# Performance work log

Hardware: AMD Instinct MI355X
Metric: run time of the kernel (lower is better)

Reference implementation:

```python
import jax, jax.numpy as jnp
import numpy as np

N = 100000

def _norm_edges(edge_index, n):
    # add self loops, compute symmetric GCN normalization
    loop = jnp.arange(n, dtype=edge_index.dtype)
    src = jnp.concatenate([edge_index[0], loop])
    dst = jnp.concatenate([edge_index[1], loop])
    deg = jax.ops.segment_sum(jnp.ones_like(dst, dtype=jnp.float32), dst, num_segments=n)
    dinv = jnp.where(deg > 0, deg ** -0.5, 0.0)
    norm = dinv[src] * dinv[dst]
    return src, dst, norm

def _gcn(x, W, b, src, dst, norm, n):
    h = x @ W  # [N, out]
    msg = h[src] * norm[:, None]
    return jax.ops.segment_sum(msg, dst, num_segments=n) + b

def setup_inputs() -> dict:
    key = jax.random.key(0)
    ks = jax.random.split(key, 20)
    E = 3200000
    d_in, d_out = 64, 64
    def w(k, i, o):
        return jax.random.normal(k, (i, o), dtype=jnp.float32) * (1.0 / np.sqrt(i))
    return {
        "x": jax.random.normal(ks[0], (N, d_in), dtype=jnp.float32),
        "t": jax.random.normal(ks[1], (N,), dtype=jnp.float32),
        "edge_index": jax.random.randint(ks[2], (2, E), 0, N, dtype=jnp.int64),
        "W1": w(ks[3], d_in + 1, 64), "b1": jnp.zeros((64,), jnp.float32),
        "W2": w(ks[4], 64, 128), "b2": jnp.zeros((128,), jnp.float32),
        "W3": w(ks[5], 128, 256), "b3": jnp.zeros((256,), jnp.float32),
        "W4": w(ks[6], 256, 128), "b4": jnp.zeros((128,), jnp.float32),
        "F1": w(ks[7], 128, 256), "c1": jnp.zeros((256,), jnp.float32),
        "F2": w(ks[8], 256, 128), "c2": jnp.zeros((128,), jnp.float32),
        "F3": w(ks[9], 128, d_out), "c3": jnp.zeros((d_out,), jnp.float32),
    }

def reference(x, t, edge_index, W1, b1, W2, b2, W3, b3, W4, b4, F1, c1, F2, c2, F3, c3):
    n = x.shape[0]
    src, dst, norm = _norm_edges(edge_index, n)
    h = jnp.concatenate([x, t[:, None]], axis=1)
    h = jax.nn.gelu(_gcn(h, W1, b1, src, dst, norm, n))
    h = jax.nn.gelu(_gcn(h, W2, b2, src, dst, norm, n))
    h = jax.nn.gelu(_gcn(h, W3, b3, src, dst, norm, n))
    h = jax.nn.gelu(_gcn(h, W4, b4, src, dst, norm, n))
    h = jax.nn.gelu(h @ F1 + c1)
    h = jax.nn.gelu(h @ F2 + c2)
    return h @ F3 + c3
```

## Files before the change

### kernel.cpp

```cpp
#include <hip/hip_runtime.h>

static constexpr int BLK = 256;

typedef double d2 __attribute__((ext_vector_type(2)));
typedef int    i4 __attribute__((ext_vector_type(4)));

__device__ __forceinline__ double gelu_d(double v){
  double u = 0.7978845608028654 * (v + 0.044715 * v * v * v);
  return 0.5 * v * (1.0 + tanh(u));
}

__global__ void zero_k(int* __restrict__ a, int n){
  int stride = gridDim.x * blockDim.x;
  for (int i = blockIdx.x*blockDim.x + threadIdx.x; i < n; i += stride) a[i] = 0;
}

__global__ void zeromax_k(unsigned long long* m){
  if (threadIdx.x == 0 && blockIdx.x == 0){
    m[0] = 0ull; m[1] = 0ull; m[2] = 0ull; m[3] = 0ull;
  }
}

__global__ void detect_k(const int* __restrict__ ei, int* __restrict__ flag){
  if (threadIdx.x == 0 && blockIdx.x == 0){
    int zeros = 0;
    for (int i = 0; i < 64; ++i) if (ei[2*i + 1] == 0) ++zeros;
    *flag = (zeros >= 48) ? 1 : 0;
  }
}

__global__ void count_k(const int* __restrict__ ei, int E, const int* __restrict__ flag,
                        int* __restrict__ cnt){
  int is64 = *flag;
  int stride = gridDim.x * blockDim.x;
  for (int e = blockIdx.x*blockDim.x + threadIdx.x; e < E; e += stride){
    int d = is64 ? ei[2*(E + e)] : ei[E + e];
    atomicAdd(&cnt[d], 1);
  }
}

__global__ void dinv_k(const int* __restrict__ cnt, double* __restrict__ dinv, int n){
  int i = blockIdx.x*blockDim.x + threadIdx.x;
  if (i < n){
    double deg = (double)(cnt[i] + 1);
    dinv[i] = 1.0 / sqrt(deg);
  }
}

__global__ __launch_bounds__(256)
void scanA_k(const int* __restrict__ cnt, int* __restrict__ partial, int n, int chunk){
  __shared__ int red[256];
  int b = blockIdx.x;
  int lo = b * chunk, hi = min(n, lo + chunk);
  int s = 0;
  for (int i = lo + threadIdx.x; i < hi; i += 256) s += cnt[i];
  red[threadIdx.x] = s; __syncthreads();
  for (int off = 128; off > 0; off >>= 1){
    if (threadIdx.x < off) red[threadIdx.x] += red[threadIdx.x + off];
    __syncthreads();
  }
  if (threadIdx.x == 0) partial[b] = red[0];
}

__global__ __launch_bounds__(256)
void scanB_k(int* __restrict__ partial, int nb){
  __shared__ int sd[256];
  int tid = threadIdx.x;
  int v = (tid < nb) ? partial[tid] : 0;
  sd[tid] = v; __syncthreads();
  for (int off = 1; off < 256; off <<= 1){
    int t = (tid >= off) ? sd[tid - off] : 0;
    __syncthreads();
    sd[tid] += t;
    __syncthreads();
  }
  if (tid < nb) partial[tid] = sd[tid] - v;
  if (tid == 255) partial[nb] = sd[255];
}

__global__ __launch_bounds__(256)
void scanC_k(const int* __restrict__ cnt, const int* __restrict__ partial,
             int* __restrict__ rp, int n, int chunk, int nb){
  __shared__ int sd[256];
  int b = blockIdx.x;
  int lo = b * chunk, hi = min(n, lo + chunk);
  int run = partial[b];
  for (int base = lo; base < hi; base += 256){
    int i = base + threadIdx.x;
    int v = (i < hi) ? cnt[i] : 0;
    sd[threadIdx.x] = v; __syncthreads();
    for (int off = 1; off < 256; off <<= 1){
      int t = (threadIdx.x >= off) ? sd[threadIdx.x - off] : 0;
      __syncthreads();
      sd[threadIdx.x] += t;
      __syncthreads();
    }
    if (i < hi) rp[i] = run + sd[threadIdx.x] - v;
    run += sd[255];
    __syncthreads();
  }
  if (b == 0 && threadIdx.x == 0) rp[n] = partial[nb];
}

__global__ void scatter_k(const int* __restrict__ ei, int E, const int* __restrict__ flag,
                          const int* __restrict__ rp, int* __restrict__ fill,
                          const double* __restrict__ dinv,
                          int* __restrict__ col, double* __restrict__ val){
  int is64 = *flag;
  int stride = gridDim.x * blockDim.x;
  for (int e = blockIdx.x*blockDim.x + threadIdx.x; e < E; e += stride){
    int s = is64 ? ei[2*e]       : ei[e];
    int d = is64 ? ei[2*(E + e)] : ei[E + e];
    int p = rp[d] + atomicAdd(&fill[d], 1);
    col[p] = s;
    if (val) val[p] = dinv[s];
  }
}

template<typename ST>
__global__ void concat_k(const float* __restrict__ x, const float* __restrict__ t,
                         ST* __restrict__ h0, int n){
  int total = n * 66;
  int stride = gridDim.x * blockDim.x;
  for (int idx = blockIdx.x*blockDim.x + threadIdx.x; idx < total; idx += stride){
    int row = idx / 66;
    int c = idx - row * 66;
    float v = (c < 64) ? x[row*64 + c] : (c == 64 ? t[row] : 0.0f);
    h0[idx] = (ST)v;
  }
}

template<typename ST>
__global__ __launch_bounds__(256, 4)
void gemm_k(const ST* __restrict__ A, int K, int lda,
            const float* __restrict__ W, int NOUT,
            const float* __restrict__ bias,
            ST* __restrict__ C, float* __restrict__ Cf,
            int n, int fuse, unsigned long long* __restrict__ amax)
{
  __shared__ __align__(16) double As[128][18];
  __shared__ __align__(16) double Ws[16][66];
  const int row0 = blockIdx.x * 128;
  const int col0 = blockIdx.y * 64;
  const int tid = threadIdx.x;
  const int tr = tid >> 4, tc = tid & 15;
  const int c0 = 2 * tc;
  double acc[8][4] = {};

  const int sar = tid >> 1;
  const int sak = (tid & 1) * 8;
  const int swr = tid >> 4;
  const int swc = (tid & 15) * 4;

  const int ktiles = (K + 15) / 16;

  double ga[8];
  float  gw[4];

  auto loadA = [&](int k0){
    int gr = row0 + sar;
    if constexpr (sizeof(ST) == 8){
      if (gr < n){
        const double* Ap = (const double*)A + (size_t)gr * lda + k0 + sak;
        #pragma unroll
        for (int g = 0; g < 4; ++g){
          d2 v = *(const d2*)(Ap + 2*g);
          ga[2*g] = v.x; ga[2*g+1] = v.y;
        }
      } else {
        #pragma unroll
        for (int u = 0; u < 8; ++u) ga[u] = 0.0;
      }
    } else {
      const ST* Ap = A + (size_t)gr * lda + k0 + sak;
      #pragma unroll
      for (int u = 0; u < 8; ++u){
        int kg = k0 + sak + u;
        ga[u] = (gr < n && kg < K) ? (double)Ap[u] : 0.0;
      }
    }
  };
  auto loadW = [&](int k0){
    int kg = k0 + swr;
    if (kg < K){
      const float* Wp = W + (size_t)kg * NOUT + col0 + swc;
      #pragma unroll
      for (int g = 0; g < 4; ++g) gw[g] = Wp[g];
    } else {
      #pragma unroll
      for (int g = 0; g < 4; ++g) gw[g] = 0.0f;
    }
  };

  loadA(0);
  loadW(0);

  for (int kt = 0; kt < ktiles; ++kt){
    #pragma unroll
    for (int g = 0; g < 4; ++g){
      d2 v; v.x = ga[2*g]; v.y = ga[2*g+1];
      *(d2*)&As[sar][sak + 2*g] = v;
    }
    {
      d2 v0; v0.x = (double)gw[0]; v0.y = (double)gw[1];
      d2 v1; v1.x = (double)gw[2]; v1.y = (double)gw[3];
      *(d2*)&Ws[swr][swc]     = v0;
      *(d2*)&Ws[swr][swc + 2] = v1;
    }
    __syncthreads();
    if (kt + 1 < ktiles){
      loadA((kt + 1) * 16);
      loadW((kt + 1) * 16);
    }
    #pragma unroll
    for (int kk = 0; kk < 16; kk += 2){
      d2 w0a = *(const d2*)&Ws[kk    ][c0];
      d2 w0b = *(const d2*)&Ws[kk    ][c0 + 32];
      d2 w1a = *(const d2*)&Ws[kk + 1][c0];
      d2 w1b = *(const d2*)&Ws[kk + 1][c0 + 32];
      #pragma unroll
      for (int i = 0; i < 8; ++i){
        d2 av = *(const d2*)&As[tr + 16*i][kk];
        acc[i][0] = fma(av.x, w0a.x, acc[i][0]);
        acc[i][1] = fma(av.x, w0a.y, acc[i][1]);
        acc[i][2] = fma(av.x, w0b.x, acc[i][2]);
        acc[i][3] = fma(av.x, w0b.y, acc[i][3]);
        acc[i][0] = fma(av.y, w1a.x, acc[i][0]);
        acc[i][1] = fma(av.y, w1a.y, acc[i][1]);
        acc[i][2] = fma(av.y, w1b.x, acc[i][2]);
        acc[i][3] = fma(av.y, w1b.y, acc[i][3]);
      }
    }
    __syncthreads();
  }
  double tmax = 0.0;
  #pragma unroll
  for (int i = 0; i < 8; ++i){
    int r = row0 + tr + 16*i;
    if (r >= n) continue;
    #pragma unroll
    for (int j = 0; j < 4; ++j){
      int c = col0 + ((j < 2) ? (c0 + j) : (c0 + 30 + j));
      double v = acc[i][j];
      if (fuse){ v += (double)bias[c]; if (fuse == 1) v = gelu_d(v); }
      if (amax) tmax = fmax(tmax, fabs(v));
      if (fuse == 2) __builtin_nontemporal_store((float)v, &Cf[(size_t)r * NOUT + c]);
      else           __builtin_nontemporal_store((ST)v,   &C [(size_t)r * NOUT + c]);
    }
  }
  if (amax){
    #pragma unroll
    for (int off = 32; off > 0; off >>= 1)
      tmax = fmax(tmax, __shfl_xor(tmax, off));
    if ((threadIdx.x & 63) == 0)
      atomicMax(amax, (unsigned long long)__double_as_longlong(tmax));
  }
}


__global__ void absmaxW_k(const float* __restrict__ W, int n, unsigned long long* __restrict__ out){
  double tmax = 0.0;
  int stride = gridDim.x * blockDim.x;
  for (int i = blockIdx.x*blockDim.x + threadIdx.x; i < n; i += stride)
    tmax = fmax(tmax, (double)fabsf(W[i]));
  #pragma unroll
  for (int off = 32; off > 0; off >>= 1)
    tmax = fmax(tmax, __shfl_xor(tmax, off));
  if ((threadIdx.x & 63) == 0)
    atomicMax(out, (unsigned long long)__double_as_longlong(tmax));
}

__global__ void quantW_k(const float* __restrict__ W, int K, int N,
                         const unsigned long long* __restrict__ maxw,
                         char* __restrict__ WqT){
  double wm = __longlong_as_double((long long)*maxw);
  int sw = (wm > 0.0) ? (37 - ilogb(wm)) : 0;
  double sc = ldexp(1.0, sw);
  int total = K * N;
  size_t NK = (size_t)N * K;
  int stride = gridDim.x * blockDim.x;
  for (int t = blockIdx.x*blockDim.x + threadIdx.x; t < total; t += stride){
    int k = t / N, nn = t - k * N;
    long long v = __double2ll_rn((double)W[t] * sc);
    #pragma unroll
    for (int p = 0; p < 5; ++p){
      int d = (int)((v + 128) & 255) - 128;
      WqT[(size_t)p * NK + (size_t)nn * K + k] = (char)d;
      v = (v - d) >> 8;
    }
  }
}

__global__ __launch_bounds__(512)
void ozaki_k(const double* __restrict__ A, const char* __restrict__ WqT,
             const unsigned long long* __restrict__ maxa,
             const unsigned long long* __restrict__ maxw,
             const float* __restrict__ bias,
             double* __restrict__ C, int n, int fuse)
{
  constexpr int K = 256, N = 128;
  constexpr int PP[22] = {0,0,0, 1,1,1,1, 2,2,2,2,2, 3,3,3,3,3, 4,4,4,4,4};
  constexpr int QQ[22] = {2,3,4, 1,2,3,4, 0,1,2,3,4, 0,1,2,3,4, 0,1,2,3,4};
  __shared__ __align__(16) char laq[5][16][272];
  const int tid  = threadIdx.x;
  const int lane = tid & 63;
  const int ct   = tid >> 6;
  const int l15  = lane & 15;
  const int lk   = lane >> 4;
  const int row0 = blockIdx.x * 16;

  double am = __longlong_as_double((long long)*maxa);
  double wm = __longlong_as_double((long long)*maxw);
  int sa = (am > 0.0) ? (38 - ilogb(am)) : 0;
  int sw = (wm > 0.0) ? (37 - ilogb(wm)) : 0;
  double sc = ldexp(1.0, sa);

  {
    int r  = tid >> 5;
    int k8 = (tid & 31) * 8;
    int gr = row0 + r; if (gr >= n) gr = n - 1;
    const double* Ap = A + (size_t)gr * K + k8;
    unsigned long long pack[5] = {0,0,0,0,0};
    #pragma unroll
    for (int u = 0; u < 8; ++u){
      long long v = __double2ll_rn(Ap[u] * sc);
      #pragma unroll
      for (int p = 0; p < 5; ++p){
        int d = (int)((v + 128) & 255) - 128;
        pack[p] |= (unsigned long long)(unsigned char)d << (8*u);
        v = (v - d) >> 8;
      }
    }
    #pragma unroll
    for (int p = 0; p < 5; ++p)
      *(unsigned long long*)&laq[p][r][k8] = pack[p];
  }
  __syncthreads();

  i4 acc[22];
  #pragma unroll
  for (int i = 0; i < 22; ++i){ i4 z = {0,0,0,0}; acc[i] = z; }

  const size_t NK = (size_t)N * K;
  const char* Wbase = WqT + (size_t)(ct * 16 + l15) * K + lk * 16;
  #pragma unroll
  for (int ks = 0; ks < 4; ++ks){
    int k0 = ks * 64;
    i4 af[5], bf[5];
    #pragma unroll
    for (int p = 0; p < 5; ++p)
      af[p] = *(const i4*)&laq[p][l15][k0 + lk*16];
    #pragma unroll
    for (int q = 0; q < 5; ++q)
      bf[q] = *(const i4*)(Wbase + (size_t)q * NK + k0);
    #pragma unroll
    for (int i = 0; i < 22; ++i)
      acc[i] = __builtin_amdgcn_mfma_i32_16x16x64_i8(af[PP[i]], bf[QQ[i]], acc[i], 0, 0, 0);
  }

  double s = ldexp(1.0, -(sa + sw));
  #pragma unroll
  for (int m = 0; m < 4; ++m){
    int r = row0 + lk * 4 + m;
    if (r >= n) continue;
    double sum = 0.0;
    #pragma unroll
    for (int i = 0; i < 22; ++i)
      sum += ldexp((double)acc[i][m], 8 * (PP[i] + QQ[i]));
    int c = ct * 16 + l15;
    double v = sum * s;
    if (fuse) v = gelu_d(v + (double)bias[c]);
    __builtin_nontemporal_store(v, &C[(size_t)r * N + c]);
  }
}

template<typename ST, int NC>
__global__ __launch_bounds__(256)
void agg_k(const ST* __restrict__ T, const int* __restrict__ rp,
           const int* __restrict__ col, const double* __restrict__ val,
           const double* __restrict__ dinv, const float* __restrict__ bias,
           ST* __restrict__ O, int n, int fuse)
{
  constexpr int DOUT = NC * 64;
  int w = (blockIdx.x * blockDim.x + threadIdx.x) >> 6;
  int lane = threadIdx.x & 63;
  if (w >= n) return;
  double dv = dinv[w];
  const ST* Ti = T + (size_t)w * DOUT;
  double acc[NC];
  #pragma unroll
  for (int c = 0; c < NC; ++c) acc[c] = dv * (double)Ti[lane + 64*c];
  int e  = rp[w];
  int e1 = rp[w + 1];
  if (val){
    for (; e + 4 <= e1; e += 4){
      int s0 = __builtin_nontemporal_load(&col[e]);
      int s1 = __builtin_nontemporal_load(&col[e+1]);
      int s2 = __builtin_nontemporal_load(&col[e+2]);
      int s3 = __builtin_nontemporal_load(&col[e+3]);
      double v0 = __builtin_nontemporal_load(&val[e]);
      double v1 = __builtin_nontemporal_load(&val[e+1]);
      double v2 = __builtin_nontemporal_load(&val[e+2]);
      double v3 = __builtin_nontemporal_load(&val[e+3]);
      const ST* T0 = T + (size_t)s0 * DOUT;
      const ST* T1 = T + (size_t)s1 * DOUT;
      const ST* T2 = T + (size_t)s2 * DOUT;
      const ST* T3 = T + (size_t)s3 * DOUT;
      double t0[NC], t1[NC], t2[NC], t3[NC];
      #pragma unroll
      for (int c = 0; c < NC; ++c){
        t0[c] = (double)T0[lane + 64*c];
        t1[c] = (double)T1[lane + 64*c];
        t2[c] = (double)T2[lane + 64*c];
        t3[c] = (double)T3[lane + 64*c];
      }
      #pragma unroll
      for (int c = 0; c < NC; ++c){
        acc[c] = fma(v0, t0[c], acc[c]);
        acc[c] = fma(v1, t1[c], acc[c]);
        acc[c] = fma(v2, t2[c], acc[c]);
        acc[c] = fma(v3, t3[c], acc[c]);
      }
    }
    for (; e < e1; ++e){
      int s = __builtin_nontemporal_load(&col[e]);
      double v = __builtin_nontemporal_load(&val[e]);
      const ST* Ts = T + (size_t)s * DOUT;
      #pragma unroll
      for (int c = 0; c < NC; ++c) acc[c] = fma(v, (double)Ts[lane + 64*c], acc[c]);
    }
  } else {
    for (; e < e1; ++e){
      int s = col[e];
      double v = dinv[s];
      const ST* Ts = T + (size_t)s * DOUT;
      #pragma unroll
      for (int c = 0; c < NC; ++c) acc[c] = fma(v, (double)Ts[lane + 64*c], acc[c]);
    }
  }
  ST* Oi = O + (size_t)w * DOUT;
  #pragma unroll
  for (int c = 0; c < NC; ++c){
    double v = dv * acc[c];
    if (fuse) v = gelu_d(v + (double)bias[lane + 64*c]);
    __builtin_nontemporal_store((ST)v, &Oi[lane + 64*c]);
  }
}

template<typename ST>
static void run_net(const float* x, const float* t,
                    const float* W1, const float* b1, const float* W2, const float* b2,
                    const float* W3, const float* b3, const float* W4, const float* b4,
                    const float* F1, const float* c1, const float* F2, const float* c2,
                    const float* F3, const float* c3,
                    ST* b256, ST* ba, ST* bb,
                    const int* rp, const int* col, const double* val, const double* dinv,
                    char* Wq4, char* WqF2, unsigned long long* maxbuf, bool ozk,
                    float* out, int N, hipStream_t stream)
{
  auto gemm = [&](const ST* A, int K, int lda, const float* W, int NOUT, const float* bias,
                  ST* C, float* Cf, int fuse, unsigned long long* amax){
    dim3 g((N + 127) / 128, NOUT / 64);
    gemm_k<ST><<<g, dim3(BLK), 0, stream>>>(A, K, lda, W, NOUT, bias, C, Cf, N, fuse, amax);
  };
  int aggGrid = (N * 64 + BLK - 1) / BLK;
  auto agg64 = [&](const ST* T, const float* bias, ST* O, int fuse){
    agg_k<ST,1><<<dim3(aggGrid), dim3(BLK), 0, stream>>>(T, rp, col, val, dinv, bias, O, N, fuse);
  };
  auto agg128 = [&](const ST* T, const float* bias, ST* O, int fuse){
    agg_k<ST,2><<<dim3(aggGrid), dim3(BLK), 0, stream>>>(T, rp, col, val, dinv, bias, O, N, fuse);
  };

  concat_k<ST><<<dim3(1024), dim3(BLK), 0, stream>>>(x, t, ba, N);
  gemm(ba, 65, 66, W1, 64, nullptr, bb, nullptr, 0, nullptr);
  agg64(bb, b1, ba, 1);
  agg64(ba, nullptr, bb, 0);
  gemm(bb, 64, 64, W2, 128, b2, ba, nullptr, 1, nullptr);
  agg128(ba, nullptr, bb, 0);
  gemm(bb, 128, 128, W3, 256, b3, b256, nullptr, 1,
       ozk ? maxbuf : nullptr);
  if (ozk){
    if constexpr (sizeof(ST) == 8){
      ozaki_k<<<dim3((N + 15) / 16), dim3(512), 0, stream>>>(
          (const double*)b256, Wq4, maxbuf, maxbuf + 1, nullptr, (double*)ba, N, 0);
    }
  } else {
    gemm(b256, 256, 256, W4, 128, nullptr, ba, nullptr, 0, nullptr);
  }
  agg128(ba, b4, bb, 1);
  gemm(bb, 128, 128, F1, 256, c1, b256, nullptr, 1,
       ozk ? maxbuf + 2 : nullptr);
  if (ozk){
    if constexpr (sizeof(ST) == 8){
      ozaki_k<<<dim3((N + 15) / 16), dim3(512), 0, stream>>>(
          (const double*)b256, WqF2, maxbuf + 2, maxbuf + 3, c2, (double*)ba, N, 1);
    }
  } else {
    gemm(b256, 256, 256, F2, 128, c2, ba, nullptr, 1, nullptr);
  }
  gemm(ba, 128, 128, F3, 64, c3, nullptr, out, 2, nullptr);
}

extern "C" void kernel_launch(void* const* d_in, const int* in_sizes, int n_in,
                              void* d_out, int out_size, void* d_ws, size_t ws_size,
                              hipStream_t stream)
{
  const float* x  = (const float*)d_in[0];
  const float* t  = (const float*)d_in[1];
  const int*   ei = (const int*)d_in[2];
  const float* W1 = (const float*)d_in[3];  const float* b1 = (const float*)d_in[4];
  const float* W2 = (const float*)d_in[5];  const float* b2 = (const float*)d_in[6];
  const float* W3 = (const float*)d_in[7];  const float* b3 = (const float*)d_in[8];
  const float* W4 = (const float*)d_in[9];  const float* b4 = (const float*)d_in[10];
  const float* F1 = (const float*)d_in[11]; const float* c1 = (const float*)d_in[12];
  const float* F2 = (const float*)d_in[13]; const float* c2 = (const float*)d_in[14];
  const float* F3 = (const float*)d_in[15]; const float* c3 = (const float*)d_in[16];
  float* out = (float*)d_out;
  int N = in_sizes[0] / 64;
  int E = in_sizes[2] / 2;

  char* p = (char*)d_ws;
  auto alloc = [&](size_t b){ char* r = p; p += (b + 255) & ~(size_t)255; return (void*)r; };
  int*    flag    = (int*)alloc(4);
  int*    cnt     = (int*)alloc((size_t)N * 4);
  int*    fill    = (int*)alloc((size_t)N * 4);
  int*    rp      = (int*)alloc((size_t)(N + 1) * 4);
  int*    partial = (int*)alloc((size_t)257 * 4);
  int*    col     = (int*)alloc((size_t)E * 4);
  double* dinv    = (double*)alloc((size_t)N * 8);
  size_t base = (size_t)(p - (char*)d_ws);

  size_t slackB = 1024;
  size_t actElems = (size_t)N * 512;
  size_t valBytes = ((size_t)E * 8 + 255) & ~(size_t)255;
  bool f64val = ws_size >= base + valBytes + actElems * sizeof(double) + 3*slackB;
  bool f64ok  = f64val || ws_size >= base + actElems * sizeof(double) + 3*slackB;
  bool f32val = ws_size >= base + valBytes + actElems * sizeof(float) + 3*slackB;
  bool f32ok  = f32val || ws_size >= base + actElems * sizeof(float) + 3*slackB;
  if (!f32ok) return;

  double* val = nullptr;
  if ((f64ok && f64val) || (!f64ok && f32val)) val = (double*)alloc((size_t)E * 8);

  int nb = 256;
  int chunk = (N + nb - 1) / nb;
  zero_k<<<dim3(256), dim3(BLK), 0, stream>>>(cnt, N);
  zero_k<<<dim3(256), dim3(BLK), 0, stream>>>(fill, N);
  detect_k<<<1, 64, 0, stream>>>(ei, flag);
  count_k<<<dim3(4096), dim3(BLK), 0, stream>>>(ei, E, flag, cnt);
  dinv_k<<<dim3((N + BLK - 1) / BLK), dim3(BLK), 0, stream>>>(cnt, dinv, N);
  scanA_k<<<dim3(nb), dim3(256), 0, stream>>>(cnt, partial, N, chunk);
  scanB_k<<<dim3(1), dim3(256), 0, stream>>>(partial, nb);
  scanC_k<<<dim3(nb), dim3(256), 0, stream>>>(cnt, partial, rp, N, chunk, nb);
  scatter_k<<<dim3(4096), dim3(BLK), 0, stream>>>(ei, E, flag, rp, fill, dinv, col, val);

  if (f64ok){
    double* b256 = (double*)alloc((size_t)N * 256 * 8 + slackB);
    double* ba   = (double*)alloc((size_t)N * 128 * 8 + slackB);
    double* bb   = (double*)alloc((size_t)N * 128 * 8 + slackB);
    size_t wqB = 5 * 128 * 256;
    size_t need = (size_t)(p - (char*)d_ws) + 2*wqB + 1024;
    bool ozk = (ws_size >= need);
    char* Wq4 = nullptr; char* WqF2 = nullptr; unsigned long long* maxbuf = nullptr;
    if (ozk){
      maxbuf = (unsigned long long*)alloc(256);
      Wq4    = (char*)alloc(wqB);
      WqF2   = (char*)alloc(wqB);
      zeromax_k<<<1, 64, 0, stream>>>(maxbuf);
      absmaxW_k<<<dim3(32), dim3(BLK), 0, stream>>>(W4, 256 * 128, maxbuf + 1);
      quantW_k<<<dim3(128), dim3(BLK), 0, stream>>>(W4, 256, 128, maxbuf + 1, Wq4);
      absmaxW_k<<<dim3(32), dim3(BLK), 0, stream>>>(F2, 256 * 128, maxbuf + 3);
      quantW_k<<<dim3(128), dim3(BLK), 0, stream>>>(F2, 256, 128, maxbuf + 3, WqF2);
    }
    run_net<double>(x, t, W1, b1, W2, b2, W3, b3, W4, b4, F1, c1, F2, c2, F3, c3,
                    b256, ba, bb, rp, col, val, dinv,
                    Wq4, WqF2, maxbuf, ozk, out, N, stream);
  } else {
    float* b256 = (float*)alloc((size_t)N * 256 * 4 + slackB);
    float* ba   = (float*)alloc((size_t)N * 128 * 4 + slackB);
    float* bb   = (float*)alloc((size_t)N * 128 * 4 + slackB);
    run_net<float>(x, t, W1, b1, W2, b2, W3, b3, W4, b4, F1, c1, F2, c2, F3, c3,
                   b256, ba, bb, rp, col, val, dinv,
                   nullptr, nullptr, nullptr, false, out, N, stream);
  }
}
```

Measured before the change: 2.560 ms.

## Extend Ozaki int8 MFMA emulation to the W3 and F1 GEMMs

```diff
diff --git a/kernel.cpp b/kernel.cpp
--- a/kernel.cpp
+++ b/kernel.cpp
@@ -16,9 +16,8 @@
 }
 
 __global__ void zeromax_k(unsigned long long* m){
-  if (threadIdx.x == 0 && blockIdx.x == 0){
-    m[0] = 0ull; m[1] = 0ull; m[2] = 0ull; m[3] = 0ull;
-  }
+  if (threadIdx.x == 0 && blockIdx.x == 0)
+    for (int i = 0; i < 8; ++i) m[i] = 0ull;
 }
 
 __global__ void detect_k(const int* __restrict__ ei, int* __restrict__ flag){
@@ -136,7 +135,7 @@
             const float* __restrict__ W, int NOUT,
             const float* __restrict__ bias,
             ST* __restrict__ C, float* __restrict__ Cf,
-            int n, int fuse, unsigned long long* __restrict__ amax)
+            int n, int fuse)
 {
   __shared__ __align__(16) double As[128][18];
   __shared__ __align__(16) double Ws[16][66];
@@ -233,7 +232,6 @@
     }
     __syncthreads();
   }
-  double tmax = 0.0;
   #pragma unroll
   for (int i = 0; i < 8; ++i){
     int r = row0 + tr + 16*i;
@@ -243,17 +241,9 @@
       int c = col0 + ((j < 2) ? (c0 + j) : (c0 + 30 + j));
       double v = acc[i][j];
       if (fuse){ v += (double)bias[c]; if (fuse == 1) v = gelu_d(v); }
-      if (amax) tmax = fmax(tmax, fabs(v));
       if (fuse == 2) __builtin_nontemporal_store((float)v, &Cf[(size_t)r * NOUT + c]);
       else           __builtin_nontemporal_store((ST)v,   &C [(size_t)r * NOUT + c]);
     }
-  }
-  if (amax){
-    #pragma unroll
-    for (int off = 32; off > 0; off >>= 1)
-      tmax = fmax(tmax, __shfl_xor(tmax, off));
-    if ((threadIdx.x & 63) == 0)
-      atomicMax(amax, (unsigned long long)__double_as_longlong(tmax));
   }
 }
 
@@ -270,11 +260,27 @@
     atomicMax(out, (unsigned long long)__double_as_longlong(tmax));
 }
 
+__global__ __launch_bounds__(256)
+void absmaxD_k(const double* __restrict__ a, size_t L, unsigned long long* __restrict__ out){
+  __shared__ double red[256];
+  double tmax = 0.0;
+  size_t stride = (size_t)gridDim.x * blockDim.x;
+  for (size_t i = blockIdx.x*(size_t)blockDim.x + threadIdx.x; i < L; i += stride)
+    tmax = fmax(tmax, fabs(a[i]));
+  red[threadIdx.x] = tmax; __syncthreads();
+  for (int off = 128; off > 0; off >>= 1){
+    if (threadIdx.x < off) red[threadIdx.x] = fmax(red[threadIdx.x], red[threadIdx.x + off]);
+    __syncthreads();
+  }
+  if (threadIdx.x == 0)
+    atomicMax(out, (unsigned long long)__double_as_longlong(red[0]));
+}
+
 __global__ void quantW_k(const float* __restrict__ W, int K, int N,
                          const unsigned long long* __restrict__ maxw,
                          char* __restrict__ WqT){
   double wm = __longlong_as_double((long long)*maxw);
-  int sw = (wm > 0.0) ? (37 - ilogb(wm)) : 0;
+  int sw = (wm > 0.0) ? (36 - ilogb(wm)) : 0;
   double sc = ldexp(1.0, sw);
   int total = K * N;
   size_t NK = (size_t)N * K;
@@ -291,49 +297,72 @@
   }
 }
 
+template<int K>
 __global__ __launch_bounds__(512)
 void ozaki_k(const double* __restrict__ A, const char* __restrict__ WqT,
              const unsigned long long* __restrict__ maxa,
              const unsigned long long* __restrict__ maxw,
              const float* __restrict__ bias,
-             double* __restrict__ C, int n, int fuse)
+             double* __restrict__ C, unsigned long long* __restrict__ amaxOut,
+             int n, int NOUT, int fuse)
 {
-  constexpr int K = 256, N = 128;
+  constexpr int PAD = 16;
   constexpr int PP[22] = {0,0,0, 1,1,1,1, 2,2,2,2,2, 3,3,3,3,3, 4,4,4,4,4};
   constexpr int QQ[22] = {2,3,4, 1,2,3,4, 0,1,2,3,4, 0,1,2,3,4, 0,1,2,3,4};
-  __shared__ __align__(16) char laq[5][16][272];
+  __shared__ __align__(16) char laq[5][16][K + PAD];
+  __shared__ double red[8];
   const int tid  = threadIdx.x;
   const int lane = tid & 63;
   const int ct   = tid >> 6;
   const int l15  = lane & 15;
   const int lk   = lane >> 4;
   const int row0 = blockIdx.x * 16;
+  const int col0g = blockIdx.y * 128;
 
   double am = __longlong_as_double((long long)*maxa);
   double wm = __longlong_as_double((long long)*maxw);
-  int sa = (am > 0.0) ? (38 - ilogb(am)) : 0;
-  int sw = (wm > 0.0) ? (37 - ilogb(wm)) : 0;
+  int sa = (am > 0.0) ? (37 - ilogb(am)) : 0;
+  int sw = (wm > 0.0) ? (36 - ilogb(wm)) : 0;
   double sc = ldexp(1.0, sa);
 
   {
-    int r  = tid >> 5;
-    int k8 = (tid & 31) * 8;
+    int r = tid >> 5;
     int gr = row0 + r; if (gr >= n) gr = n - 1;
-    const double* Ap = A + (size_t)gr * K + k8;
-    unsigned long long pack[5] = {0,0,0,0,0};
-    #pragma unroll
-    for (int u = 0; u < 8; ++u){
-      long long v = __double2ll_rn(Ap[u] * sc);
-      #pragma unroll
-      for (int p = 0; p < 5; ++p){
-        int d = (int)((v + 128) & 255) - 128;
-        pack[p] |= (unsigned long long)(unsigned char)d << (8*u);
-        v = (v - d) >> 8;
+    if constexpr (K == 256){
+      int kq = (tid & 31) * 8;
+      const double* Ap = A + (size_t)gr * K + kq;
+      unsigned long long pack[5] = {0,0,0,0,0};
+      #pragma unroll
+      for (int u = 0; u < 8; ++u){
+        long long v = __double2ll_rn(Ap[u] * sc);
+        #pragma unroll
+        for (int p = 0; p < 5; ++p){
+          int d = (int)((v + 128) & 255) - 128;
+          pack[p] |= (unsigned long long)(unsigned char)d << (8*u);
+          v = (v - d) >> 8;
+        }
       }
-    }
-    #pragma unroll
-    for (int p = 0; p < 5; ++p)
-      *(unsigned long long*)&laq[p][r][k8] = pack[p];
+      #pragma unroll
+      for (int p = 0; p < 5; ++p)
+        *(unsigned long long*)&laq[p][r][kq] = pack[p];
+    } else {
+      int kq = (tid & 31) * 4;
+      const double* Ap = A + (size_t)gr * K + kq;
+      unsigned int pack[5] = {0,0,0,0,0};
+      #pragma unroll
+      for (int u = 0; u < 4; ++u){
+        long long v = __double2ll_rn(Ap[u] * sc);
+        #pragma unroll
+        for (int p = 0; p < 5; ++p){
+          int d = (int)((v + 128) & 255) - 128;
+          pack[p] |= (unsigned int)(unsigned char)d << (8*u);
+          v = (v - d) >> 8;
+        }
+      }
+      #pragma unroll
+      for (int p = 0; p < 5; ++p)
+        *(unsigned int*)&laq[p][r][kq] = pack[p];
+    }
   }
   __syncthreads();
 
@@ -341,10 +370,10 @@
   #pragma unroll
   for (int i = 0; i < 22; ++i){ i4 z = {0,0,0,0}; acc[i] = z; }
 
-  const size_t NK = (size_t)N * K;
-  const char* Wbase = WqT + (size_t)(ct * 16 + l15) * K + lk * 16;
-  #pragma unroll
-  for (int ks = 0; ks < 4; ++ks){
+  const size_t NK = (size_t)NOUT * K;
+  const char* wb = WqT + (size_t)(col0g + ct * 16 + l15) * K + lk * 16;
+  #pragma unroll
+  for (int ks = 0; ks < K / 64; ++ks){
     int k0 = ks * 64;
     i4 af[5], bf[5];
     #pragma unroll
@@ -352,25 +381,46 @@
       af[p] = *(const i4*)&laq[p][l15][k0 + lk*16];
     #pragma unroll
     for (int q = 0; q < 5; ++q)
-      bf[q] = *(const i4*)(Wbase + (size_t)q * NK + k0);
+      bf[q] = *(const i4*)(wb + (size_t)q * NK + k0);
     #pragma unroll
     for (int i = 0; i < 22; ++i)
       acc[i] = __builtin_amdgcn_mfma_i32_16x16x64_i8(af[PP[i]], bf[QQ[i]], acc[i], 0, 0, 0);
   }
 
   double s = ldexp(1.0, -(sa + sw));
+  double w8[9];
+  #pragma unroll
+  for (int e = 2; e <= 8; ++e) w8[e] = ldexp(s, 8 * e);
+  double tmax = 0.0;
   #pragma unroll
   for (int m = 0; m < 4; ++m){
     int r = row0 + lk * 4 + m;
-    if (r >= n) continue;
+    int c = col0g + ct * 16 + l15;
+    long long g[9] = {};
+    #pragma unroll
+    for (int i = 0; i < 22; ++i) g[PP[i] + QQ[i]] += acc[i][m];
     double sum = 0.0;
     #pragma unroll
-    for (int i = 0; i < 22; ++i)
-      sum += ldexp((double)acc[i][m], 8 * (PP[i] + QQ[i]));
-    int c = ct * 16 + l15;
-    double v = sum * s;
+    for (int e = 2; e <= 8; ++e) sum = fma((double)g[e], w8[e], sum);
+    double v = sum;
     if (fuse) v = gelu_d(v + (double)bias[c]);
-    __builtin_nontemporal_store(v, &C[(size_t)r * N + c]);
+    if (r < n){
+      __builtin_nontemporal_store(v, &C[(size_t)r * NOUT + c]);
+      tmax = fmax(tmax, fabs(v));
+    }
+  }
+  if (amaxOut){
+    #pragma unroll
+    for (int off = 32; off > 0; off >>= 1)
+      tmax = fmax(tmax, __shfl_xor(tmax, off));
+    if (lane == 0) red[ct] = tmax;
+    __syncthreads();
+    if (tid == 0){
+      double mv = red[0];
+      #pragma unroll
+      for (int i = 1; i < 8; ++i) mv = fmax(mv, red[i]);
+      atomicMax(amaxOut, (unsigned long long)__double_as_longlong(mv));
+    }
   }
 }
 
@@ -455,13 +505,14 @@
                     const float* F3, const float* c3,
                     ST* b256, ST* ba, ST* bb,
                     const int* rp, const int* col, const double* val, const double* dinv,
-                    char* Wq4, char* WqF2, unsigned long long* maxbuf, bool ozk,
+                    char* Wq3, char* Wq4, char* WqF1, char* WqF2,
+                    unsigned long long* mx, bool ozk,
                     float* out, int N, hipStream_t stream)
 {
   auto gemm = [&](const ST* A, int K, int lda, const float* W, int NOUT, const float* bias,
-                  ST* C, float* Cf, int fuse, unsigned long long* amax){
+                  ST* C, float* Cf, int fuse){
     dim3 g((N + 127) / 128, NOUT / 64);
-    gemm_k<ST><<<g, dim3(BLK), 0, stream>>>(A, K, lda, W, NOUT, bias, C, Cf, N, fuse, amax);
+    gemm_k<ST><<<g, dim3(BLK), 0, stream>>>(A, K, lda, W, NOUT, bias, C, Cf, N, fuse);
   };
   int aggGrid = (N * 64 + BLK - 1) / BLK;
   auto agg64 = [&](const ST* T, const float* bias, ST* O, int fuse){
@@ -472,33 +523,35 @@
   };
 
   concat_k<ST><<<dim3(1024), dim3(BLK), 0, stream>>>(x, t, ba, N);
-  gemm(ba, 65, 66, W1, 64, nullptr, bb, nullptr, 0, nullptr);
+  gemm(ba, 65, 66, W1, 64, nullptr, bb, nullptr, 0);
   agg64(bb, b1, ba, 1);
   agg64(ba, nullptr, bb, 0);
-  gemm(bb, 64, 64, W2, 128, b2, ba, nullptr, 1, nullptr);
+  gemm(bb, 64, 64, W2, 128, b2, ba, nullptr, 1);
   agg128(ba, nullptr, bb, 0);
-  gemm(bb, 128, 128, W3, 256, b3, b256, nullptr, 1,
-       ozk ? maxbuf : nullptr);
   if (ozk){
     if constexpr (sizeof(ST) == 8){
-      ozaki_k<<<dim3((N + 15) / 16), dim3(512), 0, stream>>>(
-          (const double*)b256, Wq4, maxbuf, maxbuf + 1, nullptr, (double*)ba, N, 0);
+      double* dbb = (double*)bb; double* db256 = (double*)b256; double* dba = (double*)ba;
+      dim3 gK128((N + 15) / 16, 2), gK256((N + 15) / 16, 1);
+      absmaxD_k<<<dim3(2048), dim3(256), 0, stream>>>(dbb, (size_t)N * 128, mx + 0);
+      ozaki_k<128><<<gK128, dim3(512), 0, stream>>>(dbb, Wq3, mx + 0, mx + 1, b3,
+                                                    db256, mx + 2, N, 256, 1);
+      ozaki_k<256><<<gK256, dim3(512), 0, stream>>>(db256, Wq4, mx + 2, mx + 3, nullptr,
+                                                    dba, nullptr, N, 128, 0);
+      agg128(ba, b4, bb, 1);
+      absmaxD_k<<<dim3(2048), dim3(256), 0, stream>>>(dbb, (size_t)N * 128, mx + 4);
+      ozaki_k<128><<<gK128, dim3(512), 0, stream>>>(dbb, WqF1, mx + 4, mx + 5, c1,
+                                                    db256, mx + 6, N, 256, 1);
+      ozaki_k<256><<<gK256, dim3(512), 0, stream>>>(db256, WqF2, mx + 6, mx + 7, c2,
+                                                    dba, nullptr, N, 128, 1);
     }
   } else {
-    gemm(b256, 256, 256, W4, 128, nullptr, ba, nullptr, 0, nullptr);
-  }
-  agg128(ba, b4, bb, 1);
-  gemm(bb, 128, 128, F1, 256, c1, b256, nullptr, 1,
-       ozk ? maxbuf + 2 : nullptr);
-  if (ozk){
-    if constexpr (sizeof(ST) == 8){
-      ozaki_k<<<dim3((N + 15) / 16), dim3(512), 0, stream>>>(
-          (const double*)b256, WqF2, maxbuf + 2, maxbuf + 3, c2, (double*)ba, N, 1);
-    }
-  } else {
-    gemm(b256, 256, 256, F2, 128, c2, ba, nullptr, 1, nullptr);
-  }
-  gemm(ba, 128, 128, F3, 64, c3, nullptr, out, 2, nullptr);
+    gemm(bb, 128, 128, W3, 256, b3, b256, nullptr, 1);
+    gemm(b256, 256, 256, W4, 128, nullptr, ba, nullptr, 0);
+    agg128(ba, b4, bb, 1);
+    gemm(bb, 128, 128, F1, 256, c1, b256, nullptr, 1);
+    gemm(b256, 256, 256, F2, 128, c2, ba, nullptr, 1);
+  }
+  gemm(ba, 128, 128, F3, 64, c3, nullptr, out, 2);
 }
 
 extern "C" void kernel_launch(void* const* d_in, const int* in_sizes, int n_in,
@@ -530,17 +583,32 @@
   double* dinv    = (double*)alloc((size_t)N * 8);
   size_t base = (size_t)(p - (char*)d_ws);
 
-  size_t slackB = 1024;
-  size_t actElems = (size_t)N * 512;
+  size_t slackB   = 1024;
+  size_t actB     = (size_t)N * 512 * sizeof(double) + 3 * slackB;
+  size_t actB32   = (size_t)N * 512 * sizeof(float) + 3 * slackB;
   size_t valBytes = ((size_t)E * 8 + 255) & ~(size_t)255;
-  bool f64val = ws_size >= base + valBytes + actElems * sizeof(double) + 3*slackB;
-  bool f64ok  = f64val || ws_size >= base + actElems * sizeof(double) + 3*slackB;
-  bool f32val = ws_size >= base + valBytes + actElems * sizeof(float) + 3*slackB;
-  bool f32ok  = f32val || ws_size >= base + actElems * sizeof(float) + 3*slackB;
-  if (!f32ok) return;
+  size_t wqB      = 5 * 128 * 256;
+  size_t wqTotal  = 256 + 4 * wqB + 8 * 256;
+
+  bool ozk    = ws_size >= base + wqTotal + valBytes + actB;
+  bool f64val = ozk || ws_size >= base + valBytes + actB;
+  bool f64ok  = f64val || ws_size >= base + actB;
+  bool f32val = ws_size >= base + valBytes + actB32;
+  bool f32ok  = f32val || ws_size >= base + actB32;
+  if (!f64ok && !f32ok) return;
+
+  unsigned long long* mx = nullptr;
+  char *Wq3 = nullptr, *Wq4 = nullptr, *WqF1 = nullptr, *WqF2 = nullptr;
+  if (ozk){
+    mx   = (unsigned long long*)alloc(256);
+    Wq3  = (char*)alloc(wqB);
+    Wq4  = (char*)alloc(wqB);
+    WqF1 = (char*)alloc(wqB);
+    WqF2 = (char*)alloc(wqB);
+  }
 
   double* val = nullptr;
-  if ((f64ok && f64val) || (!f64ok && f32val)) val = (double*)alloc((size_t)E * 8);
+  if (f64ok ? f64val : f32val) val = (double*)alloc((size_t)E * 8);
 
   int nb = 256;
   int chunk = (N + nb - 1) / nb;
@@ -554,33 +622,31 @@
   scanC_k<<<dim3(nb), dim3(256), 0, stream>>>(cnt, partial, rp, N, chunk, nb);
   scatter_k<<<dim3(4096), dim3(BLK), 0, stream>>>(ei, E, flag, rp, fill, dinv, col, val);
 
+  if (ozk){
+    zeromax_k<<<1, 64, 0, stream>>>(mx);
+    absmaxW_k<<<dim3(32), dim3(BLK), 0, stream>>>(W3, 128 * 256, mx + 1);
+    quantW_k<<<dim3(128), dim3(BLK), 0, stream>>>(W3, 128, 256, mx + 1, Wq3);
+    absmaxW_k<<<dim3(32), dim3(BLK), 0, stream>>>(W4, 256 * 128, mx + 3);
+    quantW_k<<<dim3(128), dim3(BLK), 0, stream>>>(W4, 256, 128, mx + 3, Wq4);
+    absmaxW_k<<<dim3(32), dim3(BLK), 0, stream>>>(F1, 128 * 256, mx + 5);
+    quantW_k<<<dim3(128), dim3(BLK), 0, stream>>>(F1, 128, 256, mx + 5, WqF1);
+    absmaxW_k<<<dim3(32), dim3(BLK), 0, stream>>>(F2, 256 * 128, mx + 7);
+    quantW_k<<<dim3(128), dim3(BLK), 0, stream>>>(F2, 256, 128, mx + 7, WqF2);
+  }
+
   if (f64ok){
     double* b256 = (double*)alloc((size_t)N * 256 * 8 + slackB);
     double* ba   = (double*)alloc((size_t)N * 128 * 8 + slackB);
     double* bb   = (double*)alloc((size_t)N * 128 * 8 + slackB);
-    size_t wqB = 5 * 128 * 256;
-    size_t need = (size_t)(p - (char*)d_ws) + 2*wqB + 1024;
-    bool ozk = (ws_size >= need);
-    char* Wq4 = nullptr; char* WqF2 = nullptr; unsigned long long* maxbuf = nullptr;
-    if (ozk){
-      maxbuf = (unsigned long long*)alloc(256);
-      Wq4    = (char*)alloc(wqB);
-      WqF2   = (char*)alloc(wqB);
-      zeromax_k<<<1, 64, 0, stream>>>(maxbuf);
-      absmaxW_k<<<dim3(32), dim3(BLK), 0, stream>>>(W4, 256 * 128, maxbuf + 1);
-      quantW_k<<<dim3(128), dim3(BLK), 0, stream>>>(W4, 256, 128, maxbuf + 1, Wq4);
-      absmaxW_k<<<dim3(32), dim3(BLK), 0, stream>>>(F2, 256 * 128, maxbuf + 3);
-      quantW_k<<<dim3(128), dim3(BLK), 0, stream>>>(F2, 256, 128, maxbuf + 3, WqF2);
-    }
     run_net<double>(x, t, W1, b1, W2, b2, W3, b3, W4, b4, F1, c1, F2, c2, F3, c3,
                     b256, ba, bb, rp, col, val, dinv,
-                    Wq4, WqF2, maxbuf, ozk, out, N, stream);
+                    Wq3, Wq4, WqF1, WqF2, mx, ozk, out, N, stream);
   } else {
     float* b256 = (float*)alloc((size_t)N * 256 * 4 + slackB);
     float* ba   = (float*)alloc((size_t)N * 128 * 4 + slackB);
     float* bb   = (float*)alloc((size_t)N * 128 * 4 + slackB);
     run_net<float>(x, t, W1, b1, W2, b2, W3, b3, W4, b4, F1, c1, F2, c2, F3, c3,
                    b256, ba, bb, rp, col, val, dinv,
-                   nullptr, nullptr, nullptr, false, out, N, stream);
-  }
-}
+                   nullptr, nullptr, nullptr, nullptr, nullptr, false, out, N, stream);
+  }
+}
```

After: 2.543 ms. Within noise of the previous version (-0.7%).
